# Kernel tuning notes

Hardware: AMD Instinct MI355X
Metric: run time of the kernel (lower is better)

The kernel has to match this reference:

```python
import jax, jax.numpy as jnp
import numpy as np

B, A, OBS = 4096, 32, 128
E, D, H = 64, 64, 4      # gat_embed_dim, gat_hidden_dim, gat_head_num
R, NA = 256, 16          # rnn_hidden_dim, n_actions


def setup_inputs() -> dict:
    key = jax.random.key(0)
    ks = jax.random.split(key, 20)
    s = 0.05
    return {
        "inputs": jax.random.normal(ks[0], (B, A, OBS), jnp.float32),
        "hidden_state": jax.random.normal(ks[1], (B, A, R), jnp.float32),
        "mask": jax.random.randint(ks[2], (B, A, A), 0, 2, jnp.int32),
        # gat_fc: Linear(OBS -> E)
        "gat_fc_w": jax.random.normal(ks[3], (E, OBS), jnp.float32) * s,
        "gat_fc_b": jnp.zeros((E,), jnp.float32),
        # GAT layer: per-head proj E -> D, attention vectors, output proj H*D -> E
        "W_h": jax.random.normal(ks[4], (H, E, D), jnp.float32) * s,
        "a_src": jax.random.normal(ks[5], (H, D), jnp.float32) * s,
        "a_dst": jax.random.normal(ks[6], (H, D), jnp.float32) * s,
        "W_o": jax.random.normal(ks[7], (H * D, E), jnp.float32) * s,
        "b_o": jnp.zeros((E,), jnp.float32),
        # fc1: Linear(OBS+E -> R)
        "fc1_w": jax.random.normal(ks[8], (R, OBS + E), jnp.float32) * s,
        "fc1_b": jnp.zeros((R,), jnp.float32),
        # GRUCell (torch gate order r,z,n)
        "W_ih": jax.random.normal(ks[9], (3 * R, R), jnp.float32) * s,
        "W_hh": jax.random.normal(ks[10], (3 * R, R), jnp.float32) * s,
        "b_ih": jnp.zeros((3 * R,), jnp.float32),
        "b_hh": jnp.zeros((3 * R,), jnp.float32),
        # LayerNorm(R)
        "ln_g": jnp.ones((R,), jnp.float32),
        "ln_b": jnp.zeros((R,), jnp.float32),
        # fc2: Linear(R -> NA)
        "fc2_w": jax.random.normal(ks[11], (NA, R), jnp.float32) * s,
        "fc2_b": jnp.zeros((NA,), jnp.float32),
    }


def _forward(inputs, hidden_state, mask, gat_fc_w, gat_fc_b, W_h, a_src, a_dst,
             W_o, b_o, fc1_w, fc1_b, W_ih, W_hh, b_ih, b_hh, ln_g, ln_b,
             fc2_w, fc2_b):
    # ---- GAT with adjacency-masked softmax ----
    x = inputs @ gat_fc_w.T + gat_fc_b                       # [B,A,E]
    h = jnp.einsum('bae,hed->bhad', x, W_h)                  # [B,H,A,D]
    s_src = jnp.einsum('bhad,hd->bha', h, a_src)             # [B,H,A]
    s_dst = jnp.einsum('bhad,hd->bha', h, a_dst)             # [B,H,A]
    e = jax.nn.leaky_relu(s_src[..., :, None] + s_dst[..., None, :], 0.2)  # [B,H,A,A]
    e = jnp.where(mask[:, None, :, :] > 0, e, jnp.float32(-1e9))
    alpha = jax.nn.softmax(e, axis=-1)                       # [B,H,A,A]
    agg = jnp.einsum('bhij,bhjd->bhid', alpha, h)            # [B,H,A,D]
    agg = agg.transpose(0, 2, 1, 3).reshape(agg.shape[0], agg.shape[2], -1)  # [B,A,H*D]
    att = agg @ W_o + b_o                                    # [B,A,E]

    # ---- concat + fc1 + ReLU ----
    z_in = jnp.concatenate([inputs, att], axis=-1)           # [B,A,OBS+E]
    b, a, _ = z_in.shape
    z = z_in.reshape(b * a, -1)
    xr = jax.nn.relu(z @ fc1_w.T + fc1_b)                    # [B*A,R]

    # ---- GRUCell ----
    h_in = hidden_state.reshape(b * a, -1)
    gi = xr @ W_ih.T + b_ih
    gh = h_in @ W_hh.T + b_hh
    gi_r, gi_z, gi_n = jnp.split(gi, 3, axis=-1)
    gh_r, gh_z, gh_n = jnp.split(gh, 3, axis=-1)
    r = jax.nn.sigmoid(gi_r + gh_r)
    zt = jax.nn.sigmoid(gi_z + gh_z)
    n = jnp.tanh(gi_n + r * gh_n)
    hh = (1.0 - zt) * n + zt * h_in                          # [B*A,R]

    # ---- LayerNorm + fc2 ----
    mu = jnp.mean(hh, axis=-1, keepdims=True)
    var = jnp.mean(jnp.square(hh - mu), axis=-1, keepdims=True)
    hn = (hh - mu) * jax.lax.rsqrt(var + 1e-5) * ln_g + ln_b
    q = hn @ fc2_w.T + fc2_b                                 # [B*A,NA]
    return q.reshape(b, a, -1), hh.reshape(b, a, -1)


def reference(inputs, hidden_state, mask, gat_fc_w, gat_fc_b, W_h, a_src, a_dst,
              W_o, b_o, fc1_w, fc1_b, W_ih, W_hh, b_ih, b_hh, ln_g, ln_b,
              fc2_w, fc2_b):
    return _forward(inputs, hidden_state, mask, gat_fc_w, gat_fc_b, W_h, a_src,
                    a_dst, W_o, b_o, fc1_w, fc1_b, W_ih, W_hh, b_ih, b_hh,
                    ln_g, ln_b, fc2_w, fc2_b)
```

## Files before the change

### kernel.cpp

```cpp
#include <hip/hip_runtime.h>
#include <hip/hip_bf16.h>

using bf16 = __hip_bfloat16;
typedef __bf16 b8v __attribute__((ext_vector_type(8)));
typedef float  f4v __attribute__((ext_vector_type(4)));

static constexpr int  kB   = 4096;
static constexpr int  kA   = 32;
static constexpr int  kOBS = 128;
static constexpr int  kE   = 64;
static constexpr int  kD   = 64;
static constexpr int  kH   = 4;
static constexpr int  kR   = 256;
static constexpr int  kNA  = 16;
static constexpr long kT   = (long)kB * kA;

__device__ __forceinline__ float ldin(const void* p, long i, int bf) {
    return bf ? (float)((const bf16*)p)[i] : ((const float*)p)[i];
}
__device__ __forceinline__ void stout(void* p, long i, float v, int bf) {
    if (bf) ((bf16*)p)[i] = (bf16)v; else ((float*)p)[i] = v;
}
__device__ __forceinline__ unsigned short f2bu(float f) {
    bf16 b = (bf16)f;
    return __builtin_bit_cast(unsigned short, b);
}

__global__ void k_detect(const void* __restrict__ lng, int* __restrict__ flag)
{
    if (threadIdx.x == 0) {
        unsigned w = *(const unsigned*)lng;
        *flag = (w == 0x3F803F80u) ? 1 : 0;
    }
}

__global__ __launch_bounds__(128) void k0d_whx(
    const void* __restrict__ gw, const void* __restrict__ gb,
    const void* __restrict__ Wh, bf16* __restrict__ Whx,
    float* __restrict__ bh, const int* __restrict__ flag)
{
    const int isbf = *flag;
    const int n = blockIdx.x;
    const int k = threadIdx.x;
    const int head = n >> 6, d = n & 63;
    float acc = 0.f;
    for (int e = 0; e < kE; ++e)
        acc += ldin(gw, e * kOBS + k, isbf) * ldin(Wh, (head * kE + e) * kD + d, isbf);
    Whx[n * 128 + k] = (bf16)acc;
    if (k == 0) {
        float b = 0.f;
        for (int e = 0; e < kE; ++e)
            b += ldin(gb, e, isbf) * ldin(Wh, (head * kE + e) * kD + d, isbf);
        bh[n] = b;
    }
}

__global__ __launch_bounds__(256) void k0e_wcat1(
    const void* __restrict__ Wo, const void* __restrict__ bo,
    const void* __restrict__ fc1w, const void* __restrict__ fc1b,
    bf16* __restrict__ Wcat1, float* __restrict__ biasf, const int* __restrict__ flag)
{
    const int isbf = *flag;
    const int n = blockIdx.x;
    const int j = threadIdx.x;
    float acc = 0.f;
    for (int e = 0; e < kE; ++e)
        acc += ldin(Wo, j * kE + e, isbf) * ldin(fc1w, n * (kOBS + kE) + kOBS + e, isbf);
    Wcat1[n * 384 + 128 + j] = (bf16)acc;
    if (j < 128)
        Wcat1[n * 384 + j] = (bf16)ldin(fc1w, n * (kOBS + kE) + j, isbf);
    if (j == 0) {
        float b = ldin(fc1b, n, isbf);
        for (int e = 0; e < kE; ++e)
            b += ldin(fc1w, n * (kOBS + kE) + kOBS + e, isbf) * ldin(bo, e, isbf);
        biasf[n] = b;
    }
}

__global__ __launch_bounds__(256) void k0b_prep(
    const void* __restrict__ w2, const void* __restrict__ lng,
    const void* __restrict__ lnb, const void* __restrict__ b2,
    float* __restrict__ w2g, float* __restrict__ s2, float* __restrict__ c2,
    const int* __restrict__ flag)
{
    __shared__ float r1[4], r2[4];
    const int isbf = *flag;
    const int na = blockIdx.x;
    const int t  = threadIdx.x;
    float w  = ldin(w2, na * kR + t, isbf);
    float g  = ldin(lng, t, isbf);
    float lb = ldin(lnb, t, isbf);
    float wg = w * g;
    w2g[na * kR + t] = wg;
    float a = wg, b = lb * w;
#pragma unroll
    for (int o = 32; o > 0; o >>= 1) {
        a += __shfl_down(a, o);
        b += __shfl_down(b, o);
    }
    if ((t & 63) == 0) { r1[t >> 6] = a; r2[t >> 6] = b; }
    __syncthreads();
    if (t == 0) {
        s2[na] = r1[0] + r1[1] + r1[2] + r1[3];
        c2[na] = ldin(b2, na, isbf) + r2[0] + r2[1] + r2[2] + r2[3];
    }
}

__global__ __launch_bounds__(256) void k0c_wcat(
    const void* __restrict__ Wih, const void* __restrict__ Whh,
    bf16* __restrict__ Wcat, const int* __restrict__ flag)
{
    const int isbf = *flag;
    long i = (long)blockIdx.x * 256 + threadIdx.x;
    if (i >= 4L * 256 * 512) return;
    const int qq = (int)(i >> 17);
    const int n  = (int)((i >> 9) & 255);
    const int k  = (int)(i & 511);
    float v = 0.f;
    if (qq == 0)      v = (k < 256) ? ldin(Wih, n * 256 + k, isbf)         : ldin(Whh, n * 256 + (k - 256), isbf);
    else if (qq == 1) v = (k < 256) ? ldin(Wih, (256 + n) * 256 + k, isbf) : ldin(Whh, (256 + n) * 256 + (k - 256), isbf);
    else if (qq == 2) v = (k < 256) ? ldin(Wih, (512 + n) * 256 + k, isbf) : 0.f;
    else              v = (k >= 256) ? ldin(Whh, (512 + n) * 256 + (k - 256), isbf) : 0.f;
    Wcat[i] = (bf16)v;
}

__global__ __launch_bounds__(512) void k1_h(
    const void* __restrict__ inp, const bf16* __restrict__ Whx,
    const float* __restrict__ bh, bf16* __restrict__ hbuf,
    const int* __restrict__ flag)
{
    __shared__ __align__(16) unsigned char lds[49152];
    const int  isbf = *flag;
    const int  tid  = threadIdx.x;
    const int  lane = tid & 63;
    const int  l15  = lane & 15, lhi = lane >> 4;
    const int  w    = tid >> 6, wm = w >> 2, q = w & 3;
    const long m0   = (long)blockIdx.x * 128;
    const int  arow = tid >> 3, ak8 = tid & 7;

    auto swz = [](int row, int kb) -> unsigned {
        return (unsigned)(row * 128 + (kb ^ ((row & 7) << 4)));
    };

    f4v acc[4][4];
    {
        f4v zero = {0.f, 0.f, 0.f, 0.f};
#pragma unroll
        for (int i = 0; i < 4; ++i)
#pragma unroll
            for (int j = 0; j < 4; ++j) acc[i][j] = zero;
    }

    b8v ra0, ra1, rb[4];
    float4 rf0a, rf0b, rf1a, rf1b;

    auto loadA = [&](int k0) {
        const int kg = k0 * 64;
        if (isbf) {
            const bf16* ip = (const bf16*)inp;
            ra0 = *reinterpret_cast<const b8v*>(ip + (m0 + arow) * kOBS + kg + ak8 * 8);
            ra1 = *reinterpret_cast<const b8v*>(ip + (m0 + arow + 64) * kOBS + kg + ak8 * 8);
        } else {
            const float* ip = (const float*)inp;
            const float4* p0 = reinterpret_cast<const float4*>(ip + (m0 + arow) * kOBS + kg + ak8 * 8);
            const float4* p1 = reinterpret_cast<const float4*>(ip + (m0 + arow + 64) * kOBS + kg + ak8 * 8);
            rf0a = p0[0]; rf0b = p0[1];
            rf1a = p1[0]; rf1b = p1[1];
        }
    };
    auto loadB = [&](int k0) {
        const int kg = k0 * 64;
#pragma unroll
        for (int j = 0; j < 4; ++j) {
            int c = tid + 512 * j;
            int bq = c >> 9, bn = (c >> 3) & 63, bk8 = c & 7;
            rb[j] = *reinterpret_cast<const b8v*>(Whx + (bq * 64 + bn) * 128 + kg + bk8 * 8);
        }
    };
    auto writeS = [&]() {
        b8v va0, va1;
        if (isbf) { va0 = ra0; va1 = ra1; }
        else {
            union { b8v v; unsigned short u[8]; } t0, t1;
            t0.u[0] = f2bu(rf0a.x); t0.u[1] = f2bu(rf0a.y);
            t0.u[2] = f2bu(rf0a.z); t0.u[3] = f2bu(rf0a.w);
            t0.u[4] = f2bu(rf0b.x); t0.u[5] = f2bu(rf0b.y);
            t0.u[6] = f2bu(rf0b.z); t0.u[7] = f2bu(rf0b.w);
            t1.u[0] = f2bu(rf1a.x); t1.u[1] = f2bu(rf1a.y);
            t1.u[2] = f2bu(rf1a.z); t1.u[3] = f2bu(rf1a.w);
            t1.u[4] = f2bu(rf1b.x); t1.u[5] = f2bu(rf1b.y);
            t1.u[6] = f2bu(rf1b.z); t1.u[7] = f2bu(rf1b.w);
            va0 = t0.v; va1 = t1.v;
        }
        *reinterpret_cast<b8v*>(&lds[swz(arow, ak8 * 16)]) = va0;
        *reinterpret_cast<b8v*>(&lds[swz(arow + 64, ak8 * 16)]) = va1;
#pragma unroll
        for (int j = 0; j < 4; ++j) {
            int c = tid + 512 * j;
            int bq = c >> 9, bn = (c >> 3) & 63, bk8 = c & 7;
            *reinterpret_cast<b8v*>(&lds[16384u + bq * 8192u + swz(bn, bk8 * 16)]) = rb[j];
        }
    };
    auto compute = [&]() {
        const unsigned bbase = 16384u + q * 8192u;
#pragma unroll
        for (int ks = 0; ks < 2; ++ks) {
            const int kb = ks * 64 + lhi * 16;
            b8v bfr[4];
#pragma unroll
            for (int ni = 0; ni < 4; ++ni)
                bfr[ni] = *reinterpret_cast<const b8v*>(&lds[bbase + swz(ni * 16 + l15, kb)]);
#pragma unroll
            for (int mi = 0; mi < 4; ++mi) {
                b8v af = *reinterpret_cast<const b8v*>(&lds[swz(wm * 64 + mi * 16 + l15, kb)]);
#pragma unroll
                for (int ni = 0; ni < 4; ++ni)
                    acc[mi][ni] = __builtin_amdgcn_mfma_f32_16x16x32_bf16(
                        af, bfr[ni], acc[mi][ni], 0, 0, 0);
            }
        }
    };

    loadA(0); loadB(0);
#pragma unroll
    for (int k0 = 0; k0 < 2; ++k0) {
        __syncthreads();
        writeS();
        __syncthreads();
        if (k0 < 1) { loadA(1); loadB(1); }
        compute();
    }

#pragma unroll
    for (int mi = 0; mi < 4; ++mi)
#pragma unroll
        for (int ni = 0; ni < 4; ++ni) {
            const int n = q * 64 + ni * 16 + l15;
#pragma unroll
            for (int r = 0; r < 4; ++r) {
                long m = m0 + wm * 64 + mi * 16 + lhi * 4 + r;
                hbuf[m * 256 + n] = (bf16)(acc[mi][ni][r] + bh[n]);
            }
        }
}

__global__ __launch_bounds__(256) void k12_soft(
    const bf16* __restrict__ hbuf, const void* __restrict__ asrc,
    const void* __restrict__ adst, const int* __restrict__ mask,
    bf16* __restrict__ agg, const int* __restrict__ flag)
{
    __shared__ float hsm[4][32][68];
    __shared__ float al[4][32][33];
    __shared__ float ss[4][32];
    __shared__ float sd[4][32];
    const int  isbf = *flag;
    const int  tid = threadIdx.x, lane = tid & 63, hh = tid >> 6;
    const long b = blockIdx.x;

#pragma unroll
    for (int j = 0; j < 4; ++j) {
        int c = lane + j * 64;
        int t = c >> 3, d8 = c & 7;
        union { b8v v; unsigned short u[8]; } hv;
        hv.v = *reinterpret_cast<const b8v*>(hbuf + (b * 32 + t) * 256 + hh * 64 + d8 * 8);
        float4 f0, f1;
        f0.x = __uint_as_float((unsigned)hv.u[0] << 16);
        f0.y = __uint_as_float((unsigned)hv.u[1] << 16);
        f0.z = __uint_as_float((unsigned)hv.u[2] << 16);
        f0.w = __uint_as_float((unsigned)hv.u[3] << 16);
        f1.x = __uint_as_float((unsigned)hv.u[4] << 16);
        f1.y = __uint_as_float((unsigned)hv.u[5] << 16);
        f1.z = __uint_as_float((unsigned)hv.u[6] << 16);
        f1.w = __uint_as_float((unsigned)hv.u[7] << 16);
        *reinterpret_cast<float4*>(&hsm[hh][t][d8 * 8])     = f0;
        *reinterpret_cast<float4*>(&hsm[hh][t][d8 * 8 + 4]) = f1;
    }
    asm volatile("s_waitcnt lgkmcnt(0)" ::: "memory");

    {
        const int t = lane & 31;
        const void* av = (lane < 32) ? asrc : adst;
        float acc = 0.f;
#pragma unroll
        for (int d4 = 0; d4 < 16; ++d4) {
            float4 hv4 = *reinterpret_cast<const float4*>(&hsm[hh][t][d4 * 4]);
            acc += hv4.x * ldin(av, hh * kD + d4 * 4 + 0, isbf);
            acc += hv4.y * ldin(av, hh * kD + d4 * 4 + 1, isbf);
            acc += hv4.z * ldin(av, hh * kD + d4 * 4 + 2, isbf);
            acc += hv4.w * ldin(av, hh * kD + d4 * 4 + 3, isbf);
        }
        if (lane < 32) ss[hh][t] = acc; else sd[hh][t] = acc;
    }
    asm volatile("s_waitcnt lgkmcnt(0)" ::: "memory");

    {
        const int i = lane & 31, half = lane >> 5;
        const float si = ss[hh][i];
        const int* mrow = mask + (b * 32 + i) * 32 + half * 16;
        float ev[16];
        float m = -3.0e38f;
#pragma unroll
        for (int jj = 0; jj < 16; ++jj) {
            float v = si + sd[hh][half * 16 + jj];
            v = v >= 0.f ? v : 0.2f * v;
            v = (mrow[jj] > 0) ? v : -1e9f;
            ev[jj] = v;
            m = fmaxf(m, v);
        }
        m = fmaxf(m, __shfl_xor(m, 32));
        float s = 0.f;
#pragma unroll
        for (int jj = 0; jj < 16; ++jj) {
            float e = __expf(ev[jj] - m);
            ev[jj] = e; s += e;
        }
        s += __shfl_xor(s, 32);
        const float inv = 1.f / s;
#pragma unroll
        for (int jj = 0; jj < 16; ++jj)
            al[hh][i][half * 16 + jj] = ev[jj] * inv;
    }
    asm volatile("s_waitcnt lgkmcnt(0)" ::: "memory");

#pragma unroll
    for (int g = 0; g < 8; ++g) {
        int c = lane + g * 64;
        int i = c >> 4, d0 = (c & 15) * 4;
        float a0 = 0, a1 = 0, a2 = 0, a3 = 0;
        for (int j = 0; j < 32; ++j) {
            float p = al[hh][i][j];
            float4 hv4 = *reinterpret_cast<const float4*>(&hsm[hh][j][d0]);
            a0 += p * hv4.x; a1 += p * hv4.y; a2 += p * hv4.z; a3 += p * hv4.w;
        }
        ushort4 o;
        o.x = f2bu(a0); o.y = f2bu(a1); o.z = f2bu(a2); o.w = f2bu(a3);
        *reinterpret_cast<ushort4*>(agg + (b * 32 + i) * 256 + hh * 64 + d0) = o;
    }
}

__global__ __launch_bounds__(512) void k3_mfma(
    const void* __restrict__ inp, const bf16* __restrict__ agg,
    const bf16* __restrict__ Wcat1, const float* __restrict__ biasf,
    bf16* __restrict__ xr, const int* __restrict__ flag)
{
    __shared__ __align__(16) unsigned char lds[49152];
    const int  isbf = *flag;
    const int  tid  = threadIdx.x;
    const int  lane = tid & 63;
    const int  l15  = lane & 15, lhi = lane >> 4;
    const int  w    = tid >> 6, wm = w >> 2, q = w & 3;
    const long m0   = (long)blockIdx.x * 128;
    const int  arow = tid >> 3, ak8 = tid & 7;

    auto swz = [](int row, int kb) -> unsigned {
        return (unsigned)(row * 128 + (kb ^ ((row & 7) << 4)));
    };

    f4v acc[4][4];
    {
        f4v zero = {0.f, 0.f, 0.f, 0.f};
#pragma unroll
        for (int i = 0; i < 4; ++i)
#pragma unroll
            for (int j = 0; j < 4; ++j) acc[i][j] = zero;
    }

    b8v ra0, ra1, rb[4];
    float4 rf0a, rf0b, rf1a, rf1b;

    auto loadA = [&](int k0) {
        const int kg = k0 * 64;
        if (kg >= 128) {
            ra0 = *reinterpret_cast<const b8v*>(agg + (m0 + arow) * 256 + (kg - 128) + ak8 * 8);
            ra1 = *reinterpret_cast<const b8v*>(agg + (m0 + arow + 64) * 256 + (kg - 128) + ak8 * 8);
        } else if (isbf) {
            const bf16* ip = (const bf16*)inp;
            ra0 = *reinterpret_cast<const b8v*>(ip + (m0 + arow) * kOBS + kg + ak8 * 8);
            ra1 = *reinterpret_cast<const b8v*>(ip + (m0 + arow + 64) * kOBS + kg + ak8 * 8);
        } else {
            const float* ip = (const float*)inp;
            const float4* p0 = reinterpret_cast<const float4*>(ip + (m0 + arow) * kOBS + kg + ak8 * 8);
            const float4* p1 = reinterpret_cast<const float4*>(ip + (m0 + arow + 64) * kOBS + kg + ak8 * 8);
            rf0a = p0[0]; rf0b = p0[1];
            rf1a = p1[0]; rf1b = p1[1];
        }
    };
    auto loadB = [&](int k0) {
        const int kg = k0 * 64;
#pragma unroll
        for (int j = 0; j < 4; ++j) {
            int c = tid + 512 * j;
            int bq = c >> 9, bn = (c >> 3) & 63, bk8 = c & 7;
            rb[j] = *reinterpret_cast<const b8v*>(Wcat1 + ((long)(bq * 64 + bn)) * 384 + kg + bk8 * 8);
        }
    };
    auto writeS = [&](int k0) {
        const int kg = k0 * 64;
        b8v va0, va1;
        if (kg >= 128 || isbf) { va0 = ra0; va1 = ra1; }
        else {
            union { b8v v; unsigned short u[8]; } t0, t1;
            t0.u[0] = f2bu(rf0a.x); t0.u[1] = f2bu(rf0a.y);
            t0.u[2] = f2bu(rf0a.z); t0.u[3] = f2bu(rf0a.w);
            t0.u[4] = f2bu(rf0b.x); t0.u[5] = f2bu(rf0b.y);
            t0.u[6] = f2bu(rf0b.z); t0.u[7] = f2bu(rf0b.w);
            t1.u[0] = f2bu(rf1a.x); t1.u[1] = f2bu(rf1a.y);
            t1.u[2] = f2bu(rf1a.z); t1.u[3] = f2bu(rf1a.w);
            t1.u[4] = f2bu(rf1b.x); t1.u[5] = f2bu(rf1b.y);
            t1.u[6] = f2bu(rf1b.z); t1.u[7] = f2bu(rf1b.w);
            va0 = t0.v; va1 = t1.v;
        }
        *reinterpret_cast<b8v*>(&lds[swz(arow, ak8 * 16)]) = va0;
        *reinterpret_cast<b8v*>(&lds[swz(arow + 64, ak8 * 16)]) = va1;
#pragma unroll
        for (int j = 0; j < 4; ++j) {
            int c = tid + 512 * j;
            int bq = c >> 9, bn = (c >> 3) & 63, bk8 = c & 7;
            *reinterpret_cast<b8v*>(&lds[16384u + bq * 8192u + swz(bn, bk8 * 16)]) = rb[j];
        }
    };
    auto compute = [&]() {
        const unsigned bbase = 16384u + q * 8192u;
#pragma unroll
        for (int ks = 0; ks < 2; ++ks) {
            const int kb = ks * 64 + lhi * 16;
            b8v bfr[4];
#pragma unroll
            for (int ni = 0; ni < 4; ++ni)
                bfr[ni] = *reinterpret_cast<const b8v*>(&lds[bbase + swz(ni * 16 + l15, kb)]);
#pragma unroll
            for (int mi = 0; mi < 4; ++mi) {
                b8v af = *reinterpret_cast<const b8v*>(&lds[swz(wm * 64 + mi * 16 + l15, kb)]);
#pragma unroll
                for (int ni = 0; ni < 4; ++ni)
                    acc[mi][ni] = __builtin_amdgcn_mfma_f32_16x16x32_bf16(
                        af, bfr[ni], acc[mi][ni], 0, 0, 0);
            }
        }
    };

    loadA(0); loadB(0);
#pragma unroll
    for (int k0 = 0; k0 < 6; ++k0) {
        __syncthreads();
        writeS(k0);
        __syncthreads();
        if (k0 < 5) { loadA(k0 + 1); loadB(k0 + 1); }
        compute();
    }

#pragma unroll
    for (int mi = 0; mi < 4; ++mi)
#pragma unroll
        for (int ni = 0; ni < 4; ++ni) {
            const int n = q * 64 + ni * 16 + l15;
            const float bia = biasf[n];
#pragma unroll
            for (int r = 0; r < 4; ++r) {
                long m = m0 + wm * 64 + mi * 16 + lhi * 4 + r;
                xr[m * 256 + n] = (bf16)fmaxf(acc[mi][ni][r] + bia, 0.f);
            }
        }
}

__global__ __launch_bounds__(512) void k4_gru_mfma(
    const bf16* __restrict__ xr, const void* __restrict__ hprev,
    const bf16* __restrict__ Wcat,
    const void* __restrict__ bih, const void* __restrict__ bhh,
    void* __restrict__ dout, const int* __restrict__ flag)
{
    __shared__ __align__(16) unsigned char lds[49152];
    const int  isbf = *flag;
    const int  tid  = threadIdx.x;
    const int  lane = tid & 63;
    const int  l15  = lane & 15, lhi = lane >> 4;
    const int  w    = tid >> 6, wm = w >> 2, q = w & 3;
    const long m0   = (long)blockIdx.x * 128;
    const int  n0   = blockIdx.y * 64;

    const int arow = tid >> 3, ak8 = tid & 7;

    auto swz = [](int row, int kb) -> unsigned {
        return (unsigned)(row * 128 + (kb ^ ((row & 7) << 4)));
    };

    f4v acc[4][4];
    {
        f4v zero = {0.f, 0.f, 0.f, 0.f};
#pragma unroll
        for (int i = 0; i < 4; ++i)
#pragma unroll
            for (int j = 0; j < 4; ++j) acc[i][j] = zero;
    }

    b8v ra0, ra1, rb[4];
    float4 rf0a, rf0b, rf1a, rf1b;

    auto loadA = [&](int k0) {
        const int kg = k0 * 64;
        if (kg < 256) {
            ra0 = *reinterpret_cast<const b8v*>(xr + (m0 + arow) * 256 + kg + ak8 * 8);
            ra1 = *reinterpret_cast<const b8v*>(xr + (m0 + arow + 64) * 256 + kg + ak8 * 8);
        } else if (isbf) {
            const bf16* hp = (const bf16*)hprev;
            ra0 = *reinterpret_cast<const b8v*>(hp + (m0 + arow) * 256 + (kg - 256) + ak8 * 8);
            ra1 = *reinterpret_cast<const b8v*>(hp + (m0 + arow + 64) * 256 + (kg - 256) + ak8 * 8);
        } else {
            const float* hp = (const float*)hprev;
            const float4* p0 = reinterpret_cast<const float4*>(hp + (m0 + arow) * 256 + (kg - 256) + ak8 * 8);
            const float4* p1 = reinterpret_cast<const float4*>(hp + (m0 + arow + 64) * 256 + (kg - 256) + ak8 * 8);
            rf0a = p0[0]; rf0b = p0[1];
            rf1a = p1[0]; rf1b = p1[1];
        }
    };
    auto loadB = [&](int k0) {
        const int kg = k0 * 64;
#pragma unroll
        for (int j = 0; j < 4; ++j) {
            int c = tid + 512 * j;
            int bq = c >> 9, bn = (c >> 3) & 63, bk8 = c & 7;
            rb[j] = *reinterpret_cast<const b8v*>(
                Wcat + ((long)(bq * 256 + n0 + bn)) * 512 + kg + bk8 * 8);
        }
    };
    auto writeS = [&](int k0) {
        const int kg = k0 * 64;
        b8v va0, va1;
        if (kg < 256 || isbf) { va0 = ra0; va1 = ra1; }
        else {
            union { b8v v; unsigned short u[8]; } t0, t1;
            t0.u[0] = f2bu(rf0a.x); t0.u[1] = f2bu(rf0a.y);
            t0.u[2] = f2bu(rf0a.z); t0.u[3] = f2bu(rf0a.w);
            t0.u[4] = f2bu(rf0b.x); t0.u[5] = f2bu(rf0b.y);
            t0.u[6] = f2bu(rf0b.z); t0.u[7] = f2bu(rf0b.w);
            t1.u[0] = f2bu(rf1a.x); t1.u[1] = f2bu(rf1a.y);
            t1.u[2] = f2bu(rf1a.z); t1.u[3] = f2bu(rf1a.w);
            t1.u[4] = f2bu(rf1b.x); t1.u[5] = f2bu(rf1b.y);
            t1.u[6] = f2bu(rf1b.z); t1.u[7] = f2bu(rf1b.w);
            va0 = t0.v; va1 = t1.v;
        }
        *reinterpret_cast<b8v*>(&lds[swz(arow, ak8 * 16)]) = va0;
        *reinterpret_cast<b8v*>(&lds[swz(arow + 64, ak8 * 16)]) = va1;
#pragma unroll
        for (int j = 0; j < 4; ++j) {
            int c = tid + 512 * j;
            int bq = c >> 9, bn = (c >> 3) & 63, bk8 = c & 7;
            *reinterpret_cast<b8v*>(&lds[16384u + bq * 8192u + swz(bn, bk8 * 16)]) = rb[j];
        }
    };
    auto compute = [&](int k0) {
        if ((q == 2 && k0 >= 4) || (q == 3 && k0 < 4)) return;
        const unsigned bbase = 16384u + q * 8192u;
#pragma unroll
        for (int ks = 0; ks < 2; ++ks) {
            const int kb = ks * 64 + lhi * 16;
            b8v bfr[4];
#pragma unroll
            for (int ni = 0; ni < 4; ++ni)
                bfr[ni] = *reinterpret_cast<const b8v*>(&lds[bbase + swz(ni * 16 + l15, kb)]);
#pragma unroll
            for (int mi = 0; mi < 4; ++mi) {
                b8v af = *reinterpret_cast<const b8v*>(&lds[swz(wm * 64 + mi * 16 + l15, kb)]);
#pragma unroll
                for (int ni = 0; ni < 4; ++ni)
                    acc[mi][ni] = __builtin_amdgcn_mfma_f32_16x16x32_bf16(
                        af, bfr[ni], acc[mi][ni], 0, 0, 0);
            }
        }
    };

    loadA(0); loadB(0);
#pragma unroll
    for (int k0 = 0; k0 < 8; ++k0) {
        __syncthreads();
        writeS(k0);
        __syncthreads();
        if (k0 < 7) { loadA(k0 + 1); loadB(k0 + 1); }
        compute(k0);
    }

    float* ep = reinterpret_cast<float*>(lds);
#pragma unroll
    for (int mi = 0; mi < 4; ++mi) {
        __syncthreads();
#pragma unroll
        for (int ni = 0; ni < 4; ++ni)
#pragma unroll
            for (int r = 0; r < 4; ++r)
                ep[((wm * 16 + lhi * 4 + r) * 4 + q) * 68 + ni * 16 + l15] = acc[mi][ni][r];
        __syncthreads();
#pragma unroll
        for (int rep = 0; rep < 4; ++rep) {
            int o = tid + rep * 512;
            int mloc = o >> 6, nl = o & 63;
            float gr  = ep[(mloc * 4 + 0) * 68 + nl];
            float gz  = ep[(mloc * 4 + 1) * 68 + nl];
            float gin = ep[(mloc * 4 + 2) * 68 + nl];
            float ghn = ep[(mloc * 4 + 3) * 68 + nl];
            int  n = n0 + nl;
            long m = m0 + (mloc >> 4) * 64 + mi * 16 + (mloc & 15);
            float r_ = 1.f / (1.f + __expf(-(gr + ldin(bih, n, isbf) + ldin(bhh, n, isbf))));
            float z_ = 1.f / (1.f + __expf(-(gz + ldin(bih, kR + n, isbf) + ldin(bhh, kR + n, isbf))));
            float nn = tanhf(gin + ldin(bih, 2 * kR + n, isbf)
                             + r_ * (ghn + ldin(bhh, 2 * kR + n, isbf)));
            float hv = ldin(hprev, m * kR + n, isbf);
            stout(dout, kT * kNA + m * kR + n, (1.f - z_) * nn + z_ * hv, isbf);
        }
    }
}

__global__ __launch_bounds__(256) void k5_lnfc2(
    void* __restrict__ dout, const float* __restrict__ w2g,
    const float* __restrict__ s2, const float* __restrict__ c2,
    const int* __restrict__ flag)
{
    const int isbf = *flag;
    const int tid  = threadIdx.x;
    const int lane = tid & 63;
    const long t   = (long)blockIdx.x * 4 + (tid >> 6);
    const long base = kT * kNA + t * kR + lane * 4;

    float v0, v1, v2, v3;
    if (isbf) {
        const ushort4 u = *reinterpret_cast<const ushort4*>(
            (const unsigned short*)dout + base);
        v0 = __uint_as_float((unsigned)u.x << 16);
        v1 = __uint_as_float((unsigned)u.y << 16);
        v2 = __uint_as_float((unsigned)u.z << 16);
        v3 = __uint_as_float((unsigned)u.w << 16);
    } else {
        const float4 f = *reinterpret_cast<const float4*>((const float*)dout + base);
        v0 = f.x; v1 = f.y; v2 = f.z; v3 = f.w;
    }

    float s = v0 + v1 + v2 + v3;
#pragma unroll
    for (int o = 32; o > 0; o >>= 1) s += __shfl_xor(s, o);
    const float mu = s * (1.f / 256.f);
    float d0 = v0 - mu, d1 = v1 - mu, d2 = v2 - mu, d3 = v3 - mu;
    float vs = d0 * d0 + d1 * d1 + d2 * d2 + d3 * d3;
#pragma unroll
    for (int o = 32; o > 0; o >>= 1) vs += __shfl_xor(vs, o);
    const float rstd = rsqrtf(vs * (1.f / 256.f) + 1e-5f);

    const float4* wp = reinterpret_cast<const float4*>(w2g);
    float p[16];
#pragma unroll
    for (int na = 0; na < 16; ++na) {
        float4 w = wp[na * 64 + lane];
        p[na] = v0 * w.x + v1 * w.y + v2 * w.z + v3 * w.w;
    }
#pragma unroll
    for (int na = 0; na < 16; ++na) {
#pragma unroll
        for (int o = 32; o > 0; o >>= 1) p[na] += __shfl_xor(p[na], o);
    }
    if (lane < kNA) {
        float qv = rstd * (p[lane] - mu * s2[lane]) + c2[lane];
        stout(dout, t * kNA + lane, qv, isbf);
    }
}

extern "C" void kernel_launch(void* const* d_in, const int* in_sizes, int n_in,
                              void* d_out, int out_size, void* d_ws, size_t ws_size,
                              hipStream_t stream)
{
    const void* inp   = d_in[0];
    const void* hprev = d_in[1];
    const int*  mask  = (const int*)d_in[2];
    const void* gw    = d_in[3];
    const void* gb    = d_in[4];
    const void* Wh    = d_in[5];
    const void* asrc  = d_in[6];
    const void* adst  = d_in[7];
    const void* Wo    = d_in[8];
    const void* bo    = d_in[9];
    const void* fc1w  = d_in[10];
    const void* fc1b  = d_in[11];
    const void* Wih   = d_in[12];
    const void* Whh   = d_in[13];
    const void* bih   = d_in[14];
    const void* bhh   = d_in[15];
    const void* lng   = d_in[16];
    const void* lnb   = d_in[17];
    const void* w2    = d_in[18];
    const void* b2    = d_in[19];

    bf16*  agg   = (bf16*)d_ws;
    bf16*  xr    = agg + kT * 256;
    bf16*  Wcat1 = xr + kT * 256;
    float* biasf = (float*)((char*)Wcat1 + 262144);
    int*   flag  = (int*)(biasf + 256);
    bf16*  hbuf  = xr;
    bf16*  Whx   = agg;
    float* bh    = (float*)(agg + 32768);
    bf16*  Wcat  = agg;
    float* w2g   = (float*)(agg + 4 * 256 * 512);
    float* s2    = w2g + 4096;
    float* c2    = s2 + 16;

    k_detect<<<1, 64, 0, stream>>>(lng, flag);
    k0d_whx<<<256, 128, 0, stream>>>(gw, gb, Wh, Whx, bh, flag);
    k0e_wcat1<<<256, 256, 0, stream>>>(Wo, bo, fc1w, fc1b, Wcat1, biasf, flag);
    k1_h<<<kT / 128, 512, 0, stream>>>(inp, Whx, bh, hbuf, flag);
    k12_soft<<<kB, 256, 0, stream>>>(hbuf, asrc, adst, mask, agg, flag);
    k3_mfma<<<kT / 128, 512, 0, stream>>>(inp, agg, Wcat1, biasf, xr, flag);
    k0c_wcat<<<2048, 256, 0, stream>>>(Wih, Whh, Wcat, flag);
    k0b_prep<<<16, 256, 0, stream>>>(w2, lng, lnb, b2, w2g, s2, c2, flag);
    k4_gru_mfma<<<dim3(kT / 128, 4), 512, 0, stream>>>(xr, hprev, Wcat, bih, bhh, d_out, flag);
    k5_lnfc2<<<kT / 4, 256, 0, stream>>>(d_out, w2g, s2, c2, flag);
}
```

Before: 984.8 us.

## Restructure GRU MFMA so each wave holds all gates for its columns, dropping LDS epilogue

The combined GRU weight is shrunk from four zero-padded gate blocks to three dense ones (r, z and a shared n block whose input half comes from W_ih and hidden half from W_hh). Each wave now computes r, z, input-n and hidden-n accumulators for the same 16 output columns. Because of this, the gate epilogue runs directly from registers instead of going through an LDS transpose with extra barriers. Less B data is loaded and staged, LDS use drops, and idle waves in half the k-steps go away. The cost is more accumulator registers per wave and a 1D grid remap.

```diff
diff --git a/kernel.cpp b/kernel.cpp
--- a/kernel.cpp
+++ b/kernel.cpp
@@ -112,15 +112,13 @@
 {
     const int isbf = *flag;
     long i = (long)blockIdx.x * 256 + threadIdx.x;
-    if (i >= 4L * 256 * 512) return;
+    if (i >= 3L * 256 * 512) return;
     const int qq = (int)(i >> 17);
     const int n  = (int)((i >> 9) & 255);
     const int k  = (int)(i & 511);
-    float v = 0.f;
-    if (qq == 0)      v = (k < 256) ? ldin(Wih, n * 256 + k, isbf)         : ldin(Whh, n * 256 + (k - 256), isbf);
-    else if (qq == 1) v = (k < 256) ? ldin(Wih, (256 + n) * 256 + k, isbf) : ldin(Whh, (256 + n) * 256 + (k - 256), isbf);
-    else if (qq == 2) v = (k < 256) ? ldin(Wih, (512 + n) * 256 + k, isbf) : 0.f;
-    else              v = (k >= 256) ? ldin(Whh, (512 + n) * 256 + (k - 256), isbf) : 0.f;
+    const int row = qq * kR + n;
+    float v = (k < 256) ? ldin(Wih, row * 256 + k, isbf)
+                        : ldin(Whh, row * 256 + (k - 256), isbf);
     Wcat[i] = (bf16)v;
 }
 
@@ -469,14 +467,14 @@
     const void* __restrict__ bih, const void* __restrict__ bhh,
     void* __restrict__ dout, const int* __restrict__ flag)
 {
-    __shared__ __align__(16) unsigned char lds[49152];
+    __shared__ __align__(16) unsigned char lds[40960];
     const int  isbf = *flag;
     const int  tid  = threadIdx.x;
     const int  lane = tid & 63;
     const int  l15  = lane & 15, lhi = lane >> 4;
-    const int  w    = tid >> 6, wm = w >> 2, q = w & 3;
-    const long m0   = (long)blockIdx.x * 128;
-    const int  n0   = blockIdx.y * 64;
+    const int  w    = tid >> 6, wm = w >> 2, nq = w & 3;
+    const long m0   = (long)(blockIdx.x >> 2) * 128;
+    const int  n0   = (blockIdx.x & 3) * 64;
 
     const int arow = tid >> 3, ak8 = tid & 7;
 
@@ -484,16 +482,14 @@
         return (unsigned)(row * 128 + (kb ^ ((row & 7) << 4)));
     };
 
-    f4v acc[4][4];
+    f4v accr[4], accz[4], acci[4], acch[4];
     {
         f4v zero = {0.f, 0.f, 0.f, 0.f};
 #pragma unroll
-        for (int i = 0; i < 4; ++i)
-#pragma unroll
-            for (int j = 0; j < 4; ++j) acc[i][j] = zero;
-    }
-
-    b8v ra0, ra1, rb[4];
+        for (int i = 0; i < 4; ++i) { accr[i] = zero; accz[i] = zero; acci[i] = zero; acch[i] = zero; }
+    }
+
+    b8v ra0, ra1, rb[3];
     float4 rf0a, rf0b, rf1a, rf1b;
 
     auto loadA = [&](int k0) {
@@ -516,7 +512,7 @@
     auto loadB = [&](int k0) {
         const int kg = k0 * 64;
 #pragma unroll
-        for (int j = 0; j < 4; ++j) {
+        for (int j = 0; j < 3; ++j) {
             int c = tid + 512 * j;
             int bq = c >> 9, bn = (c >> 3) & 63, bk8 = c & 7;
             rb[j] = *reinterpret_cast<const b8v*>(
@@ -542,29 +538,28 @@
         *reinterpret_cast<b8v*>(&lds[swz(arow, ak8 * 16)]) = va0;
         *reinterpret_cast<b8v*>(&lds[swz(arow + 64, ak8 * 16)]) = va1;
 #pragma unroll
-        for (int j = 0; j < 4; ++j) {
+        for (int j = 0; j < 3; ++j) {
             int c = tid + 512 * j;
             int bq = c >> 9, bn = (c >> 3) & 63, bk8 = c & 7;
             *reinterpret_cast<b8v*>(&lds[16384u + bq * 8192u + swz(bn, bk8 * 16)]) = rb[j];
         }
     };
     auto compute = [&](int k0) {
-        if ((q == 2 && k0 >= 4) || (q == 3 && k0 < 4)) return;
-        const unsigned bbase = 16384u + q * 8192u;
 #pragma unroll
         for (int ks = 0; ks < 2; ++ks) {
             const int kb = ks * 64 + lhi * 16;
-            b8v bfr[4];
-#pragma unroll
-            for (int ni = 0; ni < 4; ++ni)
-                bfr[ni] = *reinterpret_cast<const b8v*>(&lds[bbase + swz(ni * 16 + l15, kb)]);
+            b8v bfr0 = *reinterpret_cast<const b8v*>(&lds[16384u + 0u * 8192u + swz(nq * 16 + l15, kb)]);
+            b8v bfr1 = *reinterpret_cast<const b8v*>(&lds[16384u + 1u * 8192u + swz(nq * 16 + l15, kb)]);
+            b8v bfr2 = *reinterpret_cast<const b8v*>(&lds[16384u + 2u * 8192u + swz(nq * 16 + l15, kb)]);
 #pragma unroll
             for (int mi = 0; mi < 4; ++mi) {
                 b8v af = *reinterpret_cast<const b8v*>(&lds[swz(wm * 64 + mi * 16 + l15, kb)]);
-#pragma unroll
-                for (int ni = 0; ni < 4; ++ni)
-                    acc[mi][ni] = __builtin_amdgcn_mfma_f32_16x16x32_bf16(
-                        af, bfr[ni], acc[mi][ni], 0, 0, 0);
+                accr[mi] = __builtin_amdgcn_mfma_f32_16x16x32_bf16(af, bfr0, accr[mi], 0, 0, 0);
+                accz[mi] = __builtin_amdgcn_mfma_f32_16x16x32_bf16(af, bfr1, accz[mi], 0, 0, 0);
+                if (k0 < 4)
+                    acci[mi] = __builtin_amdgcn_mfma_f32_16x16x32_bf16(af, bfr2, acci[mi], 0, 0, 0);
+                else
+                    acch[mi] = __builtin_amdgcn_mfma_f32_16x16x32_bf16(af, bfr2, acch[mi], 0, 0, 0);
             }
         }
     };
@@ -579,30 +574,19 @@
         compute(k0);
     }
 
-    float* ep = reinterpret_cast<float*>(lds);
+    const int n = n0 + nq * 16 + l15;
+    const float br  = ldin(bih, n, isbf)           + ldin(bhh, n, isbf);
+    const float bz  = ldin(bih, kR + n, isbf)      + ldin(bhh, kR + n, isbf);
+    const float bgi = ldin(bih, 2 * kR + n, isbf);
+    const float bgh = ldin(bhh, 2 * kR + n, isbf);
 #pragma unroll
     for (int mi = 0; mi < 4; ++mi) {
-        __syncthreads();
-#pragma unroll
-        for (int ni = 0; ni < 4; ++ni)
-#pragma unroll
-            for (int r = 0; r < 4; ++r)
-                ep[((wm * 16 + lhi * 4 + r) * 4 + q) * 68 + ni * 16 + l15] = acc[mi][ni][r];
-        __syncthreads();
-#pragma unroll
-        for (int rep = 0; rep < 4; ++rep) {
-            int o = tid + rep * 512;
-            int mloc = o >> 6, nl = o & 63;
-            float gr  = ep[(mloc * 4 + 0) * 68 + nl];
-            float gz  = ep[(mloc * 4 + 1) * 68 + nl];
-            float gin = ep[(mloc * 4 + 2) * 68 + nl];
-            float ghn = ep[(mloc * 4 + 3) * 68 + nl];
-            int  n = n0 + nl;
-            long m = m0 + (mloc >> 4) * 64 + mi * 16 + (mloc & 15);
-            float r_ = 1.f / (1.f + __expf(-(gr + ldin(bih, n, isbf) + ldin(bhh, n, isbf))));
-            float z_ = 1.f / (1.f + __expf(-(gz + ldin(bih, kR + n, isbf) + ldin(bhh, kR + n, isbf))));
-            float nn = tanhf(gin + ldin(bih, 2 * kR + n, isbf)
-                             + r_ * (ghn + ldin(bhh, 2 * kR + n, isbf)));
+#pragma unroll
+        for (int r = 0; r < 4; ++r) {
+            long m = m0 + wm * 64 + mi * 16 + lhi * 4 + r;
+            float r_ = 1.f / (1.f + __expf(-(accr[mi][r] + br)));
+            float z_ = 1.f / (1.f + __expf(-(accz[mi][r] + bz)));
+            float nn = tanhf(acci[mi][r] + bgi + r_ * (acch[mi][r] + bgh));
             float hv = ldin(hprev, m * kR + n, isbf);
             stout(dout, kT * kNA + m * kR + n, (1.f - z_) * nn + z_ * hv, isbf);
         }
@@ -705,8 +689,8 @@
     k1_h<<<kT / 128, 512, 0, stream>>>(inp, Whx, bh, hbuf, flag);
     k12_soft<<<kB, 256, 0, stream>>>(hbuf, asrc, adst, mask, agg, flag);
     k3_mfma<<<kT / 128, 512, 0, stream>>>(inp, agg, Wcat1, biasf, xr, flag);
-    k0c_wcat<<<2048, 256, 0, stream>>>(Wih, Whh, Wcat, flag);
+    k0c_wcat<<<1536, 256, 0, stream>>>(Wih, Whh, Wcat, flag);
     k0b_prep<<<16, 256, 0, stream>>>(w2, lng, lnb, b2, w2g, s2, c2, flag);
-    k4_gru_mfma<<<dim3(kT / 128, 4), 512, 0, stream>>>(xr, hprev, Wcat, bih, bhh, d_out, flag);
+    k4_gru_mfma<<<(kT / 128) * 4, 512, 0, stream>>>(xr, hprev, Wcat, bih, bhh, d_out, flag);
     k5_lnfc2<<<kT / 4, 256, 0, stream>>>(d_out, w2g, s2, c2, flag);
 }
```

Result: faster. 899.6 us (-8.6%).
